# Kernel tuning notes

Measured on AMD Instinct MI355X. Metric: run time of the kernel, lower is better.

## Reference

```python
import jax, jax.numpy as jnp
import numpy as np

EPS = 1e-5

def _layer_norm(x, gamma, beta):
    m = jnp.mean(x, axis=-1, keepdims=True)
    v = jnp.mean(jnp.square(x - m), axis=-1, keepdims=True)
    return (x - m) * jax.lax.rsqrt(v + EPS) * gamma + beta

def setup_inputs() -> dict:
    key = jax.random.key(0)
    ks = jax.random.split(key, 6)
    B, D, H = 4096, 1024, 1024
    s = 1.0 / np.sqrt(H)
    return {
        "inputs": jax.random.normal(ks[0], (B, D), jnp.float32),
        "hx": jax.random.normal(ks[1], (B, H), jnp.float32),
        "cx": jax.random.normal(ks[2], (B, H), jnp.float32),
        "w_ih": jax.random.uniform(ks[3], (4 * H, D), jnp.float32, -s, s),
        "w_hh": jax.random.uniform(ks[4], (4 * H, H), jnp.float32, -s, s),
        "b_hh": jax.random.uniform(ks[5], (4 * H,), jnp.float32, -s, s),
        "g_ih": jnp.ones((4 * H,), jnp.float32),
        "beta_ih": jnp.zeros((4 * H,), jnp.float32),
        "g_hh": jnp.ones((4 * H,), jnp.float32),
        "beta_hh": jnp.zeros((4 * H,), jnp.float32),
        "g_ho": jnp.ones((H,), jnp.float32),
        "beta_ho": jnp.zeros((H,), jnp.float32),
    }

def reference(inputs, hx, cx, w_ih, w_hh, b_hh, g_ih, beta_ih, g_hh, beta_hh, g_ho, beta_ho):
    # i2h: [B, 4H] (no input bias used in original forward)
    i2h = inputs @ w_ih.T
    h2h = hx @ w_hh.T + b_hh
    gates = _layer_norm(i2h, g_ih, beta_ih) + _layer_norm(h2h, g_hh, beta_hh)
    i, f, o, g = jnp.split(gates, 4, axis=1)  # torch chunk order: i, f, o, g
    cy = jax.nn.sigmoid(f) * cx + jax.nn.sigmoid(i) * jnp.tanh(g)
    hy = jax.nn.sigmoid(o) * _layer_norm(jnp.tanh(cy), g_ho, beta_ho)
    # Dropout(0.1) is identity in eval / deterministic reference
    return hy, cy
```

## Files before the change

kernel.cpp:

```cpp
#include <hip/hip_runtime.h>
#include <hip/hip_bf16.h>
#include <stdint.h>

typedef __attribute__((ext_vector_type(8))) short bf16x8;
typedef __attribute__((ext_vector_type(4))) float f32x4;

#define LN_EPS 1e-5f

__device__ inline unsigned f2bf(float f) {
    unsigned u = __builtin_bit_cast(unsigned, f);
    u += 0x7fffu + ((u >> 16) & 1u);
    return u >> 16;
}
__device__ inline float bf2f(unsigned u) {
    return __builtin_bit_cast(float, u << 16);
}
__device__ inline float sigf(float x) {
    return 1.0f / (1.0f + __expf(-x));
}
__device__ inline float tanh_fast(float x) {
    return __builtin_fmaf(2.0f, 1.0f / (1.0f + __expf(-2.0f * x)), -1.0f);
}
__device__ inline float wred(float v) {
#pragma unroll
    for (int o = 32; o > 0; o >>= 1) v += __shfl_xor(v, o);
    return v;
}
__device__ inline void gload_lds16(const void* g, void* l) {
    __builtin_amdgcn_global_load_lds(
        (const __attribute__((address_space(1))) void*)g,
        (__attribute__((address_space(3))) void*)l, 16, 0, 0);
}

__global__ __launch_bounds__(256) void cast_all(
    const float4* __restrict__ s0, ushort4* __restrict__ d0, int n0,
    const float4* __restrict__ s1, ushort4* __restrict__ d1, int n1,
    const float4* __restrict__ s2, ushort4* __restrict__ d2, int n2,
    const float4* __restrict__ s3, ushort4* __restrict__ d3, int n3)
{
    int j = blockIdx.x * blockDim.x + threadIdx.x;
    const float4* s; ushort4* d;
    if (j < n0) { s = s0; d = d0; }
    else {
        j -= n0;
        if (j < n1) { s = s1; d = d1; }
        else {
            j -= n1;
            if (j < n2) { s = s2; d = d2; }
            else {
                j -= n2;
                if (j >= n3) return;
                s = s3; d = d3;
            }
        }
    }
    float4 v = s[j];
    ushort4 o;
    o.x = (unsigned short)f2bf(v.x); o.y = (unsigned short)f2bf(v.y);
    o.z = (unsigned short)f2bf(v.z); o.w = (unsigned short)f2bf(v.w);
    d[j] = o;
}

#define GNT 32

__global__ __launch_bounds__(512) void gemm8p(
    const short* __restrict__ Aa, const short* __restrict__ Ba, unsigned short* __restrict__ Ca,
    const short* __restrict__ Ab, const short* __restrict__ Bb, unsigned short* __restrict__ Cb,
    const float* __restrict__ Bias,
    float2* __restrict__ P,
    int N, int K, int Bn)
{
    __shared__ __attribute__((aligned(16))) short lds[66048];
    short* ldsA = lds;
    short* ldsB = lds + 32768;
    float* biasLds = (float*)(lds + 65536);

    const int gx = gridDim.x;
    int bid = blockIdx.y * gx + blockIdx.x;
    const int cpx = (gx * gridDim.y) >> 3;
    int swz = (bid & 7) * cpx + (bid >> 3);
    const int by = swz / gx;
    const int bx = swz - by * gx;
    const int brow = by * 256, bcol = bx * 256;

    const int t    = threadIdx.x;
    const int lane = t & 63, w = t >> 6;
    const int wr = w >> 2, wc = w & 3;
    const int lr = lane & 15, kc = lane >> 4;

    const int ci0 = t, ci1 = t + 512;
    const int r0 = ci0 >> 2, l0 = (ci0 & 3) ^ ((r0 >> 1) & 3);
    const int r1 = ci1 >> 2, l1 = (ci1 & 3) ^ ((r1 >> 1) & 3);
    const int gA0 = (brow + r0) * K + l0 * 8;
    const int gA1 = (brow + r1) * K + l1 * 8;
    const int gB0 = (bcol + r0) * K + l0 * 8;
    const int gB1 = (bcol + r1) * K + l1 * 8;
    const int d0 = ci0 * 8, d1 = ci1 * 8;

#define STAGE_A(PA, u) { const int so_ = ((u) & 3) * 8192; \
    gload_lds16((PA) + gA0 + (u) * 32, ldsA + so_ + d0);   \
    gload_lds16((PA) + gA1 + (u) * 32, ldsA + so_ + d1); }
#define STAGE_B(PB, u) { const int so_ = ((u) & 3) * 8192; \
    gload_lds16((PB) + gB0 + (u) * 32, ldsB + so_ + d0);   \
    gload_lds16((PB) + gB1 + (u) * 32, ldsB + so_ + d1); }

    int offW[8], offX[4];
#pragma unroll
    for (int f = 0; f < 8; ++f) {
        int r = wr * 128 + f * 16 + lr;
        offW[f] = r * 32 + ((kc ^ ((r >> 1) & 3)) * 8);
    }
#pragma unroll
    for (int n = 0; n < 4; ++n) {
        int r = wc * 64 + n * 16 + lr;
        offX[n] = r * 32 + ((kc ^ ((r >> 1) & 3)) * 8);
    }

    if (t < 64) gload_lds16(Bias + bcol + t * 4, biasLds + t * 4);

    STAGE_A(Aa, 0); STAGE_B(Ba, 0); STAGE_A(Aa, 1); STAGE_B(Ba, 1); STAGE_A(Aa, 2);
    asm volatile("s_waitcnt vmcnt(6)" ::: "memory");
    __builtin_amdgcn_s_barrier();

    for (int zz = 0; zz < 2; ++zz) {
        const short* A = zz ? Ab : Aa;
        const short* B = zz ? Bb : Ba;
        unsigned short* C = zz ? Cb : Ca;

        f32x4 acc[8][4];
#pragma unroll
        for (int i = 0; i < 8; ++i)
#pragma unroll
            for (int j = 0; j < 4; ++j)
                acc[i][j] = (f32x4){0.f, 0.f, 0.f, 0.f};

#pragma unroll 4
        for (int T = 0; T < GNT; ++T) {
            const int so = (T & 3) * 8192;
            bf16x8 w0, w1, w2, w3, x0, x1, x2, x3;

            w0 = *(const bf16x8*)&ldsB[so + offW[0]];
            w1 = *(const bf16x8*)&ldsB[so + offW[1]];
            w2 = *(const bf16x8*)&ldsB[so + offW[2]];
            w3 = *(const bf16x8*)&ldsB[so + offW[3]];
            x0 = *(const bf16x8*)&ldsA[so + offX[0]];
            x1 = *(const bf16x8*)&ldsA[so + offX[1]];
            x2 = *(const bf16x8*)&ldsA[so + offX[2]];
            x3 = *(const bf16x8*)&ldsA[so + offX[3]];
            if (T + 2 < GNT) STAGE_B(B, T + 2);
            __builtin_amdgcn_s_barrier();
            asm volatile("s_waitcnt lgkmcnt(0)" ::: "memory");
            __builtin_amdgcn_sched_barrier(0);
            __builtin_amdgcn_s_setprio(1);
            acc[0][0] = __builtin_amdgcn_mfma_f32_16x16x32_bf16(w0, x0, acc[0][0], 0, 0, 0);
            acc[0][1] = __builtin_amdgcn_mfma_f32_16x16x32_bf16(w0, x1, acc[0][1], 0, 0, 0);
            acc[0][2] = __builtin_amdgcn_mfma_f32_16x16x32_bf16(w0, x2, acc[0][2], 0, 0, 0);
            acc[0][3] = __builtin_amdgcn_mfma_f32_16x16x32_bf16(w0, x3, acc[0][3], 0, 0, 0);
            acc[1][0] = __builtin_amdgcn_mfma_f32_16x16x32_bf16(w1, x0, acc[1][0], 0, 0, 0);
            acc[1][1] = __builtin_amdgcn_mfma_f32_16x16x32_bf16(w1, x1, acc[1][1], 0, 0, 0);
            acc[1][2] = __builtin_amdgcn_mfma_f32_16x16x32_bf16(w1, x2, acc[1][2], 0, 0, 0);
            acc[1][3] = __builtin_amdgcn_mfma_f32_16x16x32_bf16(w1, x3, acc[1][3], 0, 0, 0);
            acc[2][0] = __builtin_amdgcn_mfma_f32_16x16x32_bf16(w2, x0, acc[2][0], 0, 0, 0);
            acc[2][1] = __builtin_amdgcn_mfma_f32_16x16x32_bf16(w2, x1, acc[2][1], 0, 0, 0);
            acc[2][2] = __builtin_amdgcn_mfma_f32_16x16x32_bf16(w2, x2, acc[2][2], 0, 0, 0);
            acc[2][3] = __builtin_amdgcn_mfma_f32_16x16x32_bf16(w2, x3, acc[2][3], 0, 0, 0);
            acc[3][0] = __builtin_amdgcn_mfma_f32_16x16x32_bf16(w3, x0, acc[3][0], 0, 0, 0);
            acc[3][1] = __builtin_amdgcn_mfma_f32_16x16x32_bf16(w3, x1, acc[3][1], 0, 0, 0);
            acc[3][2] = __builtin_amdgcn_mfma_f32_16x16x32_bf16(w3, x2, acc[3][2], 0, 0, 0);
            acc[3][3] = __builtin_amdgcn_mfma_f32_16x16x32_bf16(w3, x3, acc[3][3], 0, 0, 0);
            __builtin_amdgcn_s_setprio(0);
            __builtin_amdgcn_s_barrier();

            w0 = *(const bf16x8*)&ldsB[so + offW[4]];
            w1 = *(const bf16x8*)&ldsB[so + offW[5]];
            w2 = *(const bf16x8*)&ldsB[so + offW[6]];
            w3 = *(const bf16x8*)&ldsB[so + offW[7]];
            if (T + 3 < GNT) STAGE_A(A, T + 3);
            __builtin_amdgcn_s_barrier();
            asm volatile("s_waitcnt lgkmcnt(0)" ::: "memory");
            __builtin_amdgcn_sched_barrier(0);
            __builtin_amdgcn_s_setprio(1);
            acc[4][0] = __builtin_amdgcn_mfma_f32_16x16x32_bf16(w0, x0, acc[4][0], 0, 0, 0);
            acc[4][1] = __builtin_amdgcn_mfma_f32_16x16x32_bf16(w0, x1, acc[4][1], 0, 0, 0);
            acc[4][2] = __builtin_amdgcn_mfma_f32_16x16x32_bf16(w0, x2, acc[4][2], 0, 0, 0);
            acc[4][3] = __builtin_amdgcn_mfma_f32_16x16x32_bf16(w0, x3, acc[4][3], 0, 0, 0);
            acc[5][0] = __builtin_amdgcn_mfma_f32_16x16x32_bf16(w1, x0, acc[5][0], 0, 0, 0);
            acc[5][1] = __builtin_amdgcn_mfma_f32_16x16x32_bf16(w1, x1, acc[5][1], 0, 0, 0);
            acc[5][2] = __builtin_amdgcn_mfma_f32_16x16x32_bf16(w1, x2, acc[5][2], 0, 0, 0);
            acc[5][3] = __builtin_amdgcn_mfma_f32_16x16x32_bf16(w1, x3, acc[5][3], 0, 0, 0);
            acc[6][0] = __builtin_amdgcn_mfma_f32_16x16x32_bf16(w2, x0, acc[6][0], 0, 0, 0);
            acc[6][1] = __builtin_amdgcn_mfma_f32_16x16x32_bf16(w2, x1, acc[6][1], 0, 0, 0);
            acc[6][2] = __builtin_amdgcn_mfma_f32_16x16x32_bf16(w2, x2, acc[6][2], 0, 0, 0);
            acc[6][3] = __builtin_amdgcn_mfma_f32_16x16x32_bf16(w2, x3, acc[6][3], 0, 0, 0);
            acc[7][0] = __builtin_amdgcn_mfma_f32_16x16x32_bf16(w3, x0, acc[7][0], 0, 0, 0);
            acc[7][1] = __builtin_amdgcn_mfma_f32_16x16x32_bf16(w3, x1, acc[7][1], 0, 0, 0);
            acc[7][2] = __builtin_amdgcn_mfma_f32_16x16x32_bf16(w3, x2, acc[7][2], 0, 0, 0);
            acc[7][3] = __builtin_amdgcn_mfma_f32_16x16x32_bf16(w3, x3, acc[7][3], 0, 0, 0);
            __builtin_amdgcn_s_setprio(0);
            if (T < GNT - 3)      { asm volatile("s_waitcnt vmcnt(6)" ::: "memory"); }
            else if (T == GNT - 3){ asm volatile("s_waitcnt vmcnt(4)" ::: "memory"); }
            else if (T == GNT - 2){ asm volatile("s_waitcnt vmcnt(0)" ::: "memory"); }
            __builtin_amdgcn_s_barrier();
        }

        if (zz == 0) {
            STAGE_A(Ab, 0); STAGE_B(Bb, 0); STAGE_A(Ab, 1); STAGE_B(Bb, 1); STAGE_A(Ab, 2);
        }

        const int gc0 = bcol + wr * 128 + kc * 4;
        const int mr0 = brow + wc * 64 + lr;
        const int bl0 = wr * 32 + kc;

        float s[4] = {0.f, 0.f, 0.f, 0.f}, q[4] = {0.f, 0.f, 0.f, 0.f};
#pragma unroll
        for (int f = 0; f < 8; ++f) {
            float4 b4;
            if (zz) b4 = ((const float4*)biasLds)[bl0 + f * 4];
            else    b4 = (float4){0.f, 0.f, 0.f, 0.f};
#pragma unroll
            for (int n = 0; n < 4; ++n) {
                float v0 = acc[f][n][0] + b4.x;
                float v1 = acc[f][n][1] + b4.y;
                float v2 = acc[f][n][2] + b4.z;
                float v3 = acc[f][n][3] + b4.w;
                unsigned u0 = f2bf(v0), u1 = f2bf(v1), u2 = f2bf(v2), u3 = f2bf(v3);
                float e0 = bf2f(u0), e1 = bf2f(u1), e2 = bf2f(u2), e3 = bf2f(u3);
                s[n] += (e0 + e1) + (e2 + e3);
                q[n] += (e0 * e0 + e1 * e1) + (e2 * e2 + e3 * e3);
                uint2 pk; pk.x = u0 | (u1 << 16); pk.y = u2 | (u3 << 16);
                *reinterpret_cast<uint2*>(&C[(size_t)(mr0 + n * 16) * N + gc0 + f * 16]) = pk;
            }
        }
#pragma unroll
        for (int n = 0; n < 4; ++n) {
            s[n] += __shfl_xor(s[n], 16); s[n] += __shfl_xor(s[n], 32);
            q[n] += __shfl_xor(q[n], 16); q[n] += __shfl_xor(q[n], 32);
        }
        if (kc == 0) {
#pragma unroll
            for (int n = 0; n < 4; ++n) {
                float2 pr; pr.x = s[n]; pr.y = q[n];
                P[(size_t)(zz * Bn + mr0 + n * 16) * 32 + bx * 2 + wr] = pr;
            }
        }

        if (zz == 0) {
            asm volatile("s_waitcnt vmcnt(0)" ::: "memory");
            __builtin_amdgcn_s_barrier();
        }
    }
#undef STAGE_A
#undef STAGE_B
}

__global__ __launch_bounds__(256) void ln_lstm(
    const unsigned short* __restrict__ i2h,
    const unsigned short* __restrict__ h2h,
    const float* __restrict__ cx,
    const float2* __restrict__ P,
    const float* __restrict__ g_ih, const float* __restrict__ be_ih,
    const float* __restrict__ g_hh, const float* __restrict__ be_hh,
    const float* __restrict__ g_ho, const float* __restrict__ be_ho,
    float* __restrict__ hy, float* __restrict__ cy, int H, int B)
{
    const int b = blockIdx.x;
    const int t = threadIdx.x;
    const int lane = t & 63;
    const int wave = t >> 6;
    const int H4 = 4 * H;
    const int h0 = t * 4;

    const unsigned short* xi = i2h + (size_t)b * H4;
    const unsigned short* xh = h2h + (size_t)b * H4;

    __shared__ float red[4][2];
    __shared__ float st[4];

    if (wave == 0) {
        const int half = lane >> 5;
        float2 v = P[((size_t)half * B + b) * 32 + (lane & 31)];
        v.x += __shfl_xor(v.x, 1);  v.y += __shfl_xor(v.y, 1);
        v.x += __shfl_xor(v.x, 2);  v.y += __shfl_xor(v.y, 2);
        v.x += __shfl_xor(v.x, 4);  v.y += __shfl_xor(v.y, 4);
        v.x += __shfl_xor(v.x, 8);  v.y += __shfl_xor(v.y, 8);
        v.x += __shfl_xor(v.x, 16); v.y += __shfl_xor(v.y, 16);
        if ((lane & 31) == 0) {
            const float inv4H = 1.0f / (float)H4;
            float m = v.x * inv4H;
            float r = rsqrtf(v.y * inv4H - m * m + LN_EPS);
            st[half * 2]     = m;
            st[half * 2 + 1] = r;
        }
    }
    __syncthreads();
    const float mI = st[0], rI = st[1], mH = st[2], rH = st[3];

    float gate[4][4];
#pragma unroll
    for (int q = 0; q < 4; ++q) {
        const int j = q * H + h0;
        ushort4 vi = *reinterpret_cast<const ushort4*>(&xi[j]);
        ushort4 vh = *reinterpret_cast<const ushort4*>(&xh[j]);
        float4 gi = *reinterpret_cast<const float4*>(&g_ih[j]);
        float4 bi = *reinterpret_cast<const float4*>(&be_ih[j]);
        float4 gh = *reinterpret_cast<const float4*>(&g_hh[j]);
        float4 bh = *reinterpret_cast<const float4*>(&be_hh[j]);
        gate[q][0] = (bf2f(vi.x) - mI) * rI * gi.x + bi.x + (bf2f(vh.x) - mH) * rH * gh.x + bh.x;
        gate[q][1] = (bf2f(vi.y) - mI) * rI * gi.y + bi.y + (bf2f(vh.y) - mH) * rH * gh.y + bh.y;
        gate[q][2] = (bf2f(vi.z) - mI) * rI * gi.z + bi.z + (bf2f(vh.z) - mH) * rH * gh.z + bh.z;
        gate[q][3] = (bf2f(vi.w) - mI) * rI * gi.w + bi.w + (bf2f(vh.w) - mH) * rH * gh.w + bh.w;
    }

    float4 cxv = *reinterpret_cast<const float4*>(&cx[(size_t)b * H + h0]);
    float cvals[4] = {cxv.x, cxv.y, cxv.z, cxv.w};
    float tv[4], ov[4];
    float s2 = 0.f, q2 = 0.f;
    float4 cyv;
#pragma unroll
    for (int k = 0; k < 4; ++k) {
        float c = sigf(gate[1][k]) * cvals[k] + sigf(gate[0][k]) * tanh_fast(gate[3][k]);
        ((float*)&cyv)[k] = c;
        float tc = tanh_fast(c);
        tv[k] = tc; ov[k] = sigf(gate[2][k]);
        s2 += tc; q2 += tc * tc;
    }
    *reinterpret_cast<float4*>(&cy[(size_t)b * H + h0]) = cyv;

    s2 = wred(s2); q2 = wred(q2);
    if (lane == 0) { red[wave][0] = s2; red[wave][1] = q2; }
    __syncthreads();
    float S2 = red[0][0] + red[1][0] + red[2][0] + red[3][0];
    float Q2 = red[0][1] + red[1][1] + red[2][1] + red[3][1];
    const float invH = 1.0f / (float)H;
    float mt = S2 * invH;
    float rt = rsqrtf(Q2 * invH - mt * mt + LN_EPS);

    float4 go = *reinterpret_cast<const float4*>(&g_ho[h0]);
    float4 bo = *reinterpret_cast<const float4*>(&be_ho[h0]);
    float4 hyv;
    hyv.x = ov[0] * ((tv[0] - mt) * rt * go.x + bo.x);
    hyv.y = ov[1] * ((tv[1] - mt) * rt * go.y + bo.y);
    hyv.z = ov[2] * ((tv[2] - mt) * rt * go.z + bo.z);
    hyv.w = ov[3] * ((tv[3] - mt) * rt * go.w + bo.w);
    *reinterpret_cast<float4*>(&hy[(size_t)b * H + h0]) = hyv;
}

extern "C" void kernel_launch(void* const* d_in, const int* in_sizes, int n_in,
                              void* d_out, int out_size, void* d_ws, size_t ws_size,
                              hipStream_t stream) {
    const float* inputs  = (const float*)d_in[0];
    const float* hx      = (const float*)d_in[1];
    const float* cx      = (const float*)d_in[2];
    const float* w_ih    = (const float*)d_in[3];
    const float* w_hh    = (const float*)d_in[4];
    const float* b_hh    = (const float*)d_in[5];
    const float* g_ih    = (const float*)d_in[6];
    const float* beta_ih = (const float*)d_in[7];
    const float* g_hh    = (const float*)d_in[8];
    const float* beta_hh = (const float*)d_in[9];
    const float* g_ho    = (const float*)d_in[10];
    const float* beta_ho = (const float*)d_in[11];

    const int H  = in_sizes[10];
    const int B  = in_sizes[1] / H;
    const int D  = in_sizes[0] / B;
    const int H4 = 4 * H;

    uint8_t* ws = (uint8_t*)d_ws;
    size_t off = 0;
    short* Abf  = (short*)(ws + off); off += (size_t)B * D * 2;
    short* Hbf  = (short*)(ws + off); off += (size_t)B * H * 2;
    short* Wih  = (short*)(ws + off); off += (size_t)H4 * D * 2;
    short* Whh  = (short*)(ws + off); off += (size_t)H4 * H * 2;
    unsigned short* i2hb = (unsigned short*)(ws + off); off += (size_t)B * H4 * 2;
    unsigned short* h2hb = (unsigned short*)(ws + off); off += (size_t)B * H4 * 2;
    float2* P   = (float2*)(ws + off); off += (size_t)2 * B * 32 * sizeof(float2);

    float* hy  = (float*)d_out;
    float* cyo = (float*)d_out + (size_t)B * H;

    {
        const int n0 = (B * D) / 4, n1 = (B * H) / 4, n2 = (H4 * D) / 4, n3 = (H4 * H) / 4;
        const int tot = n0 + n1 + n2 + n3;
        cast_all<<<(tot + 255) / 256, 256, 0, stream>>>(
            (const float4*)inputs, (ushort4*)Abf, n0,
            (const float4*)hx,     (ushort4*)Hbf, n1,
            (const float4*)w_ih,   (ushort4*)Wih, n2,
            (const float4*)w_hh,   (ushort4*)Whh, n3);
    }

    {
        dim3 grid(H4 / 256, B / 256, 1);
        gemm8p<<<grid, 512, 0, stream>>>(Abf, Wih, i2hb, Hbf, Whh, h2hb, b_hh, P, H4, D, B);
    }

    ln_lstm<<<B, 256, 0, stream>>>(i2hb, h2hb, cx, P,
                                   g_ih, beta_ih, g_hh, beta_hh, g_ho, beta_ho,
                                   hy, cyo, H, B);
}
```

Baseline: 134.6 us.

## Split dual GEMM across grid z and fold bias into padded K column

```diff
diff --git a/kernel.cpp b/kernel.cpp
--- a/kernel.cpp
+++ b/kernel.cpp
@@ -6,6 +6,8 @@
 typedef __attribute__((ext_vector_type(4))) float f32x4;
 
 #define LN_EPS 1e-5f
+#define KP 1056
+#define GNT 33
 
 __device__ inline unsigned f2bf(float f) {
     unsigned u = __builtin_bit_cast(unsigned, f);
@@ -32,55 +34,71 @@
         (__attribute__((address_space(3))) void*)l, 16, 0, 0);
 }
 
-__global__ __launch_bounds__(256) void cast_all(
-    const float4* __restrict__ s0, ushort4* __restrict__ d0, int n0,
-    const float4* __restrict__ s1, ushort4* __restrict__ d1, int n1,
-    const float4* __restrict__ s2, ushort4* __restrict__ d2, int n2,
-    const float4* __restrict__ s3, ushort4* __restrict__ d3, int n3)
+__global__ __launch_bounds__(256) void cast_aug(
+    const float* __restrict__ inputs, const float* __restrict__ hx,
+    const float* __restrict__ w_ih,   const float* __restrict__ w_hh,
+    const float* __restrict__ b_hh,
+    unsigned short* __restrict__ Abf, unsigned short* __restrict__ Hbf,
+    unsigned short* __restrict__ Wih, unsigned short* __restrict__ Whh)
 {
+    const int CPR = 132;
+    const int PERREG = 4096 * CPR;
     int j = blockIdx.x * blockDim.x + threadIdx.x;
-    const float4* s; ushort4* d;
-    if (j < n0) { s = s0; d = d0; }
-    else {
-        j -= n0;
-        if (j < n1) { s = s1; d = d1; }
-        else {
-            j -= n1;
-            if (j < n2) { s = s2; d = d2; }
-            else {
-                j -= n2;
-                if (j >= n3) return;
-                s = s3; d = d3;
-            }
+    const int r = j / PERREG;
+    if (r >= 4) return;
+    const int rem = j - r * PERREG;
+    const int row = rem / CPR;
+    const int c8  = rem - row * CPR;
+
+    const float* src; unsigned short* dst;
+    switch (r) {
+        case 0: src = inputs; dst = Abf; break;
+        case 1: src = hx;     dst = Hbf; break;
+        case 2: src = w_ih;   dst = Wih; break;
+        default: src = w_hh;  dst = Whh; break;
+    }
+
+    uint4 v;
+    if (c8 < 128) {
+        const float4* sp = reinterpret_cast<const float4*>(src + (size_t)row * 1024 + c8 * 8);
+        float4 a = sp[0], b = sp[1];
+        v.x = f2bf(a.x) | (f2bf(a.y) << 16);
+        v.y = f2bf(a.z) | (f2bf(a.w) << 16);
+        v.z = f2bf(b.x) | (f2bf(b.y) << 16);
+        v.w = f2bf(b.z) | (f2bf(b.w) << 16);
+    } else {
+        v.x = v.y = v.z = v.w = 0u;
+        if (c8 == 128) {
+            if (r == 1) v.x = 0x3F80u;
+            else if (r == 3) v.x = f2bf(b_hh[row]);
         }
     }
-    float4 v = s[j];
-    ushort4 o;
-    o.x = (unsigned short)f2bf(v.x); o.y = (unsigned short)f2bf(v.y);
-    o.z = (unsigned short)f2bf(v.z); o.w = (unsigned short)f2bf(v.w);
-    d[j] = o;
-}
-
-#define GNT 32
+    *reinterpret_cast<uint4*>(dst + (size_t)row * KP + c8 * 8) = v;
+}
 
 __global__ __launch_bounds__(512) void gemm8p(
-    const short* __restrict__ Aa, const short* __restrict__ Ba, unsigned short* __restrict__ Ca,
-    const short* __restrict__ Ab, const short* __restrict__ Bb, unsigned short* __restrict__ Cb,
-    const float* __restrict__ Bias,
+    const unsigned short* __restrict__ Aa, const unsigned short* __restrict__ Ba, unsigned short* __restrict__ Ca,
+    const unsigned short* __restrict__ Ab, const unsigned short* __restrict__ Bb, unsigned short* __restrict__ Cb,
     float2* __restrict__ P,
-    int N, int K, int Bn)
+    int N, int Bn)
 {
-    __shared__ __attribute__((aligned(16))) short lds[66048];
+    __shared__ __attribute__((aligned(16))) short lds[65536];
     short* ldsA = lds;
     short* ldsB = lds + 32768;
-    float* biasLds = (float*)(lds + 65536);
-
-    const int gx = gridDim.x;
-    int bid = blockIdx.y * gx + blockIdx.x;
-    const int cpx = (gx * gridDim.y) >> 3;
+
+    const int gx  = gridDim.x;
+    const int gxy = gx * gridDim.y;
+    int bid = (blockIdx.z * gridDim.y + blockIdx.y) * gx + blockIdx.x;
+    const int cpx = (gxy * gridDim.z) >> 3;
     int swz = (bid & 7) * cpx + (bid >> 3);
-    const int by = swz / gx;
-    const int bx = swz - by * gx;
+    const int z  = swz / gxy;
+    const int r2 = swz - z * gxy;
+    const int by = r2 / gx;
+    const int bx = r2 - by * gx;
+
+    const unsigned short* __restrict__ A = z ? Ab : Aa;
+    const unsigned short* __restrict__ B = z ? Bb : Ba;
+    unsigned short* __restrict__ C = z ? Cb : Ca;
     const int brow = by * 256, bcol = bx * 256;
 
     const int t    = threadIdx.x;
@@ -91,18 +109,18 @@
     const int ci0 = t, ci1 = t + 512;
     const int r0 = ci0 >> 2, l0 = (ci0 & 3) ^ ((r0 >> 1) & 3);
     const int r1 = ci1 >> 2, l1 = (ci1 & 3) ^ ((r1 >> 1) & 3);
-    const int gA0 = (brow + r0) * K + l0 * 8;
-    const int gA1 = (brow + r1) * K + l1 * 8;
-    const int gB0 = (bcol + r0) * K + l0 * 8;
-    const int gB1 = (bcol + r1) * K + l1 * 8;
+    const int gA0 = (brow + r0) * KP + l0 * 8;
+    const int gA1 = (brow + r1) * KP + l1 * 8;
+    const int gB0 = (bcol + r0) * KP + l0 * 8;
+    const int gB1 = (bcol + r1) * KP + l1 * 8;
     const int d0 = ci0 * 8, d1 = ci1 * 8;
 
-#define STAGE_A(PA, u) { const int so_ = ((u) & 3) * 8192; \
-    gload_lds16((PA) + gA0 + (u) * 32, ldsA + so_ + d0);   \
-    gload_lds16((PA) + gA1 + (u) * 32, ldsA + so_ + d1); }
-#define STAGE_B(PB, u) { const int so_ = ((u) & 3) * 8192; \
-    gload_lds16((PB) + gB0 + (u) * 32, ldsB + so_ + d0);   \
-    gload_lds16((PB) + gB1 + (u) * 32, ldsB + so_ + d1); }
+#define STAGE_A(u) { const int so_ = ((u) & 3) * 8192; \
+    gload_lds16(A + gA0 + (u) * 32, ldsA + so_ + d0);  \
+    gload_lds16(A + gA1 + (u) * 32, ldsA + so_ + d1); }
+#define STAGE_B(u) { const int so_ = ((u) & 3) * 8192; \
+    gload_lds16(B + gB0 + (u) * 32, ldsB + so_ + d0);  \
+    gload_lds16(B + gB1 + (u) * 32, ldsB + so_ + d1); }
 
     int offW[8], offX[4];
 #pragma unroll
@@ -116,137 +134,113 @@
         offX[n] = r * 32 + ((kc ^ ((r >> 1) & 3)) * 8);
     }
 
-    if (t < 64) gload_lds16(Bias + bcol + t * 4, biasLds + t * 4);
-
-    STAGE_A(Aa, 0); STAGE_B(Ba, 0); STAGE_A(Aa, 1); STAGE_B(Ba, 1); STAGE_A(Aa, 2);
+    f32x4 acc[8][4];
+#pragma unroll
+    for (int i = 0; i < 8; ++i)
+#pragma unroll
+        for (int j = 0; j < 4; ++j)
+            acc[i][j] = (f32x4){0.f, 0.f, 0.f, 0.f};
+
+    STAGE_A(0); STAGE_B(0); STAGE_A(1); STAGE_B(1); STAGE_A(2);
     asm volatile("s_waitcnt vmcnt(6)" ::: "memory");
     __builtin_amdgcn_s_barrier();
 
-    for (int zz = 0; zz < 2; ++zz) {
-        const short* A = zz ? Ab : Aa;
-        const short* B = zz ? Bb : Ba;
-        unsigned short* C = zz ? Cb : Ca;
-
-        f32x4 acc[8][4];
-#pragma unroll
-        for (int i = 0; i < 8; ++i)
-#pragma unroll
-            for (int j = 0; j < 4; ++j)
-                acc[i][j] = (f32x4){0.f, 0.f, 0.f, 0.f};
-
 #pragma unroll 4
-        for (int T = 0; T < GNT; ++T) {
-            const int so = (T & 3) * 8192;
-            bf16x8 w0, w1, w2, w3, x0, x1, x2, x3;
-
-            w0 = *(const bf16x8*)&ldsB[so + offW[0]];
-            w1 = *(const bf16x8*)&ldsB[so + offW[1]];
-            w2 = *(const bf16x8*)&ldsB[so + offW[2]];
-            w3 = *(const bf16x8*)&ldsB[so + offW[3]];
-            x0 = *(const bf16x8*)&ldsA[so + offX[0]];
-            x1 = *(const bf16x8*)&ldsA[so + offX[1]];
-            x2 = *(const bf16x8*)&ldsA[so + offX[2]];
-            x3 = *(const bf16x8*)&ldsA[so + offX[3]];
-            if (T + 2 < GNT) STAGE_B(B, T + 2);
-            __builtin_amdgcn_s_barrier();
-            asm volatile("s_waitcnt lgkmcnt(0)" ::: "memory");
-            __builtin_amdgcn_sched_barrier(0);
-            __builtin_amdgcn_s_setprio(1);
-            acc[0][0] = __builtin_amdgcn_mfma_f32_16x16x32_bf16(w0, x0, acc[0][0], 0, 0, 0);
-            acc[0][1] = __builtin_amdgcn_mfma_f32_16x16x32_bf16(w0, x1, acc[0][1], 0, 0, 0);
-            acc[0][2] = __builtin_amdgcn_mfma_f32_16x16x32_bf16(w0, x2, acc[0][2], 0, 0, 0);
-            acc[0][3] = __builtin_amdgcn_mfma_f32_16x16x32_bf16(w0, x3, acc[0][3], 0, 0, 0);
-            acc[1][0] = __builtin_amdgcn_mfma_f32_16x16x32_bf16(w1, x0, acc[1][0], 0, 0, 0);
-            acc[1][1] = __builtin_amdgcn_mfma_f32_16x16x32_bf16(w1, x1, acc[1][1], 0, 0, 0);
-            acc[1][2] = __builtin_amdgcn_mfma_f32_16x16x32_bf16(w1, x2, acc[1][2], 0, 0, 0);
-            acc[1][3] = __builtin_amdgcn_mfma_f32_16x16x32_bf16(w1, x3, acc[1][3], 0, 0, 0);
-            acc[2][0] = __builtin_amdgcn_mfma_f32_16x16x32_bf16(w2, x0, acc[2][0], 0, 0, 0);
-            acc[2][1] = __builtin_amdgcn_mfma_f32_16x16x32_bf16(w2, x1, acc[2][1], 0, 0, 0);
-            acc[2][2] = __builtin_amdgcn_mfma_f32_16x16x32_bf16(w2, x2, acc[2][2], 0, 0, 0);
-            acc[2][3] = __builtin_amdgcn_mfma_f32_16x16x32_bf16(w2, x3, acc[2][3], 0, 0, 0);
-            acc[3][0] = __builtin_amdgcn_mfma_f32_16x16x32_bf16(w3, x0, acc[3][0], 0, 0, 0);
-            acc[3][1] = __builtin_amdgcn_mfma_f32_16x16x32_bf16(w3, x1, acc[3][1], 0, 0, 0);
-            acc[3][2] = __builtin_amdgcn_mfma_f32_16x16x32_bf16(w3, x2, acc[3][2], 0, 0, 0);
-            acc[3][3] = __builtin_amdgcn_mfma_f32_16x16x32_bf16(w3, x3, acc[3][3], 0, 0, 0);
-            __builtin_amdgcn_s_setprio(0);
-            __builtin_amdgcn_s_barrier();
-
-            w0 = *(const bf16x8*)&ldsB[so + offW[4]];
-            w1 = *(const bf16x8*)&ldsB[so + offW[5]];
-            w2 = *(const bf16x8*)&ldsB[so + offW[6]];
-            w3 = *(const bf16x8*)&ldsB[so + offW[7]];
-            if (T + 3 < GNT) STAGE_A(A, T + 3);
-            __builtin_amdgcn_s_barrier();
-            asm volatile("s_waitcnt lgkmcnt(0)" ::: "memory");
-            __builtin_amdgcn_sched_barrier(0);
-            __builtin_amdgcn_s_setprio(1);
-            acc[4][0] = __builtin_amdgcn_mfma_f32_16x16x32_bf16(w0, x0, acc[4][0], 0, 0, 0);
-            acc[4][1] = __builtin_amdgcn_mfma_f32_16x16x32_bf16(w0, x1, acc[4][1], 0, 0, 0);
-            acc[4][2] = __builtin_amdgcn_mfma_f32_16x16x32_bf16(w0, x2, acc[4][2], 0, 0, 0);
-            acc[4][3] = __builtin_amdgcn_mfma_f32_16x16x32_bf16(w0, x3, acc[4][3], 0, 0, 0);
-            acc[5][0] = __builtin_amdgcn_mfma_f32_16x16x32_bf16(w1, x0, acc[5][0], 0, 0, 0);
-            acc[5][1] = __builtin_amdgcn_mfma_f32_16x16x32_bf16(w1, x1, acc[5][1], 0, 0, 0);
-            acc[5][2] = __builtin_amdgcn_mfma_f32_16x16x32_bf16(w1, x2, acc[5][2], 0, 0, 0);
-            acc[5][3] = __builtin_amdgcn_mfma_f32_16x16x32_bf16(w1, x3, acc[5][3], 0, 0, 0);
-            acc[6][0] = __builtin_amdgcn_mfma_f32_16x16x32_bf16(w2, x0, acc[6][0], 0, 0, 0);
-            acc[6][1] = __builtin_amdgcn_mfma_f32_16x16x32_bf16(w2, x1, acc[6][1], 0, 0, 0);
-            acc[6][2] = __builtin_amdgcn_mfma_f32_16x16x32_bf16(w2, x2, acc[6][2], 0, 0, 0);
-            acc[6][3] = __builtin_amdgcn_mfma_f32_16x16x32_bf16(w2, x3, acc[6][3], 0, 0, 0);
-            acc[7][0] = __builtin_amdgcn_mfma_f32_16x16x32_bf16(w3, x0, acc[7][0], 0, 0, 0);
-            acc[7][1] = __builtin_amdgcn_mfma_f32_16x16x32_bf16(w3, x1, acc[7][1], 0, 0, 0);
-            acc[7][2] = __builtin_amdgcn_mfma_f32_16x16x32_bf16(w3, x2, acc[7][2], 0, 0, 0);
-            acc[7][3] = __builtin_amdgcn_mfma_f32_16x16x32_bf16(w3, x3, acc[7][3], 0, 0, 0);
-            __builtin_amdgcn_s_setprio(0);
-            if (T < GNT - 3)      { asm volatile("s_waitcnt vmcnt(6)" ::: "memory"); }
-            else if (T == GNT - 3){ asm volatile("s_waitcnt vmcnt(4)" ::: "memory"); }
-            else if (T == GNT - 2){ asm volatile("s_waitcnt vmcnt(0)" ::: "memory"); }
-            __builtin_amdgcn_s_barrier();
+    for (int T = 0; T < GNT; ++T) {
+        const int so = (T & 3) * 8192;
+        bf16x8 w0, w1, w2, w3, x0, x1, x2, x3;
+
+        w0 = *(const bf16x8*)&ldsB[so + offW[0]];
+        w1 = *(const bf16x8*)&ldsB[so + offW[1]];
+        w2 = *(const bf16x8*)&ldsB[so + offW[2]];
+        w3 = *(const bf16x8*)&ldsB[so + offW[3]];
+        x0 = *(const bf16x8*)&ldsA[so + offX[0]];
+        x1 = *(const bf16x8*)&ldsA[so + offX[1]];
+        x2 = *(const bf16x8*)&ldsA[so + offX[2]];
+        x3 = *(const bf16x8*)&ldsA[so + offX[3]];
+        if (T + 2 < GNT) STAGE_B(T + 2);
+        __builtin_amdgcn_s_barrier();
+        asm volatile("s_waitcnt lgkmcnt(0)" ::: "memory");
+        __builtin_amdgcn_sched_barrier(0);
+        __builtin_amdgcn_s_setprio(1);
+        acc[0][0] = __builtin_amdgcn_mfma_f32_16x16x32_bf16(w0, x0, acc[0][0], 0, 0, 0);
+        acc[0][1] = __builtin_amdgcn_mfma_f32_16x16x32_bf16(w0, x1, acc[0][1], 0, 0, 0);
+        acc[0][2] = __builtin_amdgcn_mfma_f32_16x16x32_bf16(w0, x2, acc[0][2], 0, 0, 0);
+        acc[0][3] = __builtin_amdgcn_mfma_f32_16x16x32_bf16(w0, x3, acc[0][3], 0, 0, 0);
+        acc[1][0] = __builtin_amdgcn_mfma_f32_16x16x32_bf16(w1, x0, acc[1][0], 0, 0, 0);
+        acc[1][1] = __builtin_amdgcn_mfma_f32_16x16x32_bf16(w1, x1, acc[1][1], 0, 0, 0);
+        acc[1][2] = __builtin_amdgcn_mfma_f32_16x16x32_bf16(w1, x2, acc[1][2], 0, 0, 0);
+        acc[1][3] = __builtin_amdgcn_mfma_f32_16x16x32_bf16(w1, x3, acc[1][3], 0, 0, 0);
+        acc[2][0] = __builtin_amdgcn_mfma_f32_16x16x32_bf16(w2, x0, acc[2][0], 0, 0, 0);
+        acc[2][1] = __builtin_amdgcn_mfma_f32_16x16x32_bf16(w2, x1, acc[2][1], 0, 0, 0);
+        acc[2][2] = __builtin_amdgcn_mfma_f32_16x16x32_bf16(w2, x2, acc[2][2], 0, 0, 0);
+        acc[2][3] = __builtin_amdgcn_mfma_f32_16x16x32_bf16(w2, x3, acc[2][3], 0, 0, 0);
+        acc[3][0] = __builtin_amdgcn_mfma_f32_16x16x32_bf16(w3, x0, acc[3][0], 0, 0, 0);
+        acc[3][1] = __builtin_amdgcn_mfma_f32_16x16x32_bf16(w3, x1, acc[3][1], 0, 0, 0);
+        acc[3][2] = __builtin_amdgcn_mfma_f32_16x16x32_bf16(w3, x2, acc[3][2], 0, 0, 0);
+        acc[3][3] = __builtin_amdgcn_mfma_f32_16x16x32_bf16(w3, x3, acc[3][3], 0, 0, 0);
+        __builtin_amdgcn_s_setprio(0);
+        __builtin_amdgcn_s_barrier();
+
+        w0 = *(const bf16x8*)&ldsB[so + offW[4]];
+        w1 = *(const bf16x8*)&ldsB[so + offW[5]];
+        w2 = *(const bf16x8*)&ldsB[so + offW[6]];
+        w3 = *(const bf16x8*)&ldsB[so + offW[7]];
+        if (T + 3 < GNT) STAGE_A(T + 3);
+        __builtin_amdgcn_s_barrier();
+        asm volatile("s_waitcnt lgkmcnt(0)" ::: "memory");
+        __builtin_amdgcn_sched_barrier(0);
+        __builtin_amdgcn_s_setprio(1);
+        acc[4][0] = __builtin_amdgcn_mfma_f32_16x16x32_bf16(w0, x0, acc[4][0], 0, 0, 0);
+        acc[4][1] = __builtin_amdgcn_mfma_f32_16x16x32_bf16(w0, x1, acc[4][1], 0, 0, 0);
+        acc[4][2] = __builtin_amdgcn_mfma_f32_16x16x32_bf16(w0, x2, acc[4][2], 0, 0, 0);
+        acc[4][3] = __builtin_amdgcn_mfma_f32_16x16x32_bf16(w0, x3, acc[4][3], 0, 0, 0);
+        acc[5][0] = __builtin_amdgcn_mfma_f32_16x16x32_bf16(w1, x0, acc[5][0], 0, 0, 0);
+        acc[5][1] = __builtin_amdgcn_mfma_f32_16x16x32_bf16(w1, x1, acc[5][1], 0, 0, 0);
+        acc[5][2] = __builtin_amdgcn_mfma_f32_16x16x32_bf16(w1, x2, acc[5][2], 0, 0, 0);
+        acc[5][3] = __builtin_amdgcn_mfma_f32_16x16x32_bf16(w1, x3, acc[5][3], 0, 0, 0);
+        acc[6][0] = __builtin_amdgcn_mfma_f32_16x16x32_bf16(w2, x0, acc[6][0], 0, 0, 0);
+        acc[6][1] = __builtin_amdgcn_mfma_f32_16x16x32_bf16(w2, x1, acc[6][1], 0, 0, 0);
+        acc[6][2] = __builtin_amdgcn_mfma_f32_16x16x32_bf16(w2, x2, acc[6][2], 0, 0, 0);
+        acc[6][3] = __builtin_amdgcn_mfma_f32_16x16x32_bf16(w2, x3, acc[6][3], 0, 0, 0);
+        acc[7][0] = __builtin_amdgcn_mfma_f32_16x16x32_bf16(w3, x0, acc[7][0], 0, 0, 0);
+        acc[7][1] = __builtin_amdgcn_mfma_f32_16x16x32_bf16(w3, x1, acc[7][1], 0, 0, 0);
+        acc[7][2] = __builtin_amdgcn_mfma_f32_16x16x32_bf16(w3, x2, acc[7][2], 0, 0, 0);
+        acc[7][3] = __builtin_amdgcn_mfma_f32_16x16x32_bf16(w3, x3, acc[7][3], 0, 0, 0);
+        __builtin_amdgcn_s_setprio(0);
+        if (T < GNT - 3)      { asm volatile("s_waitcnt vmcnt(6)" ::: "memory"); }
+        else if (T == GNT - 3){ asm volatile("s_waitcnt vmcnt(4)" ::: "memory"); }
+        else if (T == GNT - 2){ asm volatile("s_waitcnt vmcnt(0)" ::: "memory"); }
+        __builtin_amdgcn_s_barrier();
+    }
+
+    const int gc0 = bcol + wr * 128 + kc * 4;
+    const int mr0 = brow + wc * 64 + lr;
+
+    float s[4] = {0.f, 0.f, 0.f, 0.f}, q[4] = {0.f, 0.f, 0.f, 0.f};
+#pragma unroll
+    for (int f = 0; f < 8; ++f) {
+#pragma unroll
+        for (int n = 0; n < 4; ++n) {
+            float a0 = acc[f][n][0], a1 = acc[f][n][1];
+            float a2 = acc[f][n][2], a3 = acc[f][n][3];
+            s[n] += (a0 + a1) + (a2 + a3);
+            q[n] += __builtin_fmaf(a0, a0, a1 * a1) + __builtin_fmaf(a2, a2, a3 * a3);
+            unsigned u0 = f2bf(a0), u1 = f2bf(a1), u2 = f2bf(a2), u3 = f2bf(a3);
+            uint2 pk; pk.x = u0 | (u1 << 16); pk.y = u2 | (u3 << 16);
+            *reinterpret_cast<uint2*>(&C[(size_t)(mr0 + n * 16) * N + gc0 + f * 16]) = pk;
         }
-
-        if (zz == 0) {
-            STAGE_A(Ab, 0); STAGE_B(Bb, 0); STAGE_A(Ab, 1); STAGE_B(Bb, 1); STAGE_A(Ab, 2);
-        }
-
-        const int gc0 = bcol + wr * 128 + kc * 4;
-        const int mr0 = brow + wc * 64 + lr;
-        const int bl0 = wr * 32 + kc;
-
-        float s[4] = {0.f, 0.f, 0.f, 0.f}, q[4] = {0.f, 0.f, 0.f, 0.f};
-#pragma unroll
-        for (int f = 0; f < 8; ++f) {
-            float4 b4;
-            if (zz) b4 = ((const float4*)biasLds)[bl0 + f * 4];
-            else    b4 = (float4){0.f, 0.f, 0.f, 0.f};
-#pragma unroll
-            for (int n = 0; n < 4; ++n) {
-                float v0 = acc[f][n][0] + b4.x;
-                float v1 = acc[f][n][1] + b4.y;
-                float v2 = acc[f][n][2] + b4.z;
-                float v3 = acc[f][n][3] + b4.w;
-                unsigned u0 = f2bf(v0), u1 = f2bf(v1), u2 = f2bf(v2), u3 = f2bf(v3);
-                float e0 = bf2f(u0), e1 = bf2f(u1), e2 = bf2f(u2), e3 = bf2f(u3);
-                s[n] += (e0 + e1) + (e2 + e3);
-                q[n] += (e0 * e0 + e1 * e1) + (e2 * e2 + e3 * e3);
-                uint2 pk; pk.x = u0 | (u1 << 16); pk.y = u2 | (u3 << 16);
-                *reinterpret_cast<uint2*>(&C[(size_t)(mr0 + n * 16) * N + gc0 + f * 16]) = pk;
-            }
-        }
+    }
+#pragma unroll
+    for (int n = 0; n < 4; ++n) {
+        s[n] += __shfl_xor(s[n], 16); s[n] += __shfl_xor(s[n], 32);
+        q[n] += __shfl_xor(q[n], 16); q[n] += __shfl_xor(q[n], 32);
+    }
+    if (kc == 0) {
 #pragma unroll
         for (int n = 0; n < 4; ++n) {
-            s[n] += __shfl_xor(s[n], 16); s[n] += __shfl_xor(s[n], 32);
-            q[n] += __shfl_xor(q[n], 16); q[n] += __shfl_xor(q[n], 32);
-        }
-        if (kc == 0) {
-#pragma unroll
-            for (int n = 0; n < 4; ++n) {
-                float2 pr; pr.x = s[n]; pr.y = q[n];
-                P[(size_t)(zz * Bn + mr0 + n * 16) * 32 + bx * 2 + wr] = pr;
-            }
-        }
-
-        if (zz == 0) {
-            asm volatile("s_waitcnt vmcnt(0)" ::: "memory");
-            __builtin_amdgcn_s_barrier();
+            float2 pr; pr.x = s[n]; pr.y = q[n];
+            P[(size_t)(z * Bn + mr0 + n * 16) * 32 + bx * 2 + wr] = pr;
         }
     }
 #undef STAGE_A
@@ -363,15 +357,14 @@
 
     const int H  = in_sizes[10];
     const int B  = in_sizes[1] / H;
-    const int D  = in_sizes[0] / B;
     const int H4 = 4 * H;
 
     uint8_t* ws = (uint8_t*)d_ws;
     size_t off = 0;
-    short* Abf  = (short*)(ws + off); off += (size_t)B * D * 2;
-    short* Hbf  = (short*)(ws + off); off += (size_t)B * H * 2;
-    short* Wih  = (short*)(ws + off); off += (size_t)H4 * D * 2;
-    short* Whh  = (short*)(ws + off); off += (size_t)H4 * H * 2;
+    unsigned short* Abf = (unsigned short*)(ws + off); off += (size_t)B * KP * 2;
+    unsigned short* Hbf = (unsigned short*)(ws + off); off += (size_t)B * KP * 2;
+    unsigned short* Wih = (unsigned short*)(ws + off); off += (size_t)H4 * KP * 2;
+    unsigned short* Whh = (unsigned short*)(ws + off); off += (size_t)H4 * KP * 2;
     unsigned short* i2hb = (unsigned short*)(ws + off); off += (size_t)B * H4 * 2;
     unsigned short* h2hb = (unsigned short*)(ws + off); off += (size_t)B * H4 * 2;
     float2* P   = (float2*)(ws + off); off += (size_t)2 * B * 32 * sizeof(float2);
@@ -380,18 +373,14 @@
     float* cyo = (float*)d_out + (size_t)B * H;
 
     {
-        const int n0 = (B * D) / 4, n1 = (B * H) / 4, n2 = (H4 * D) / 4, n3 = (H4 * H) / 4;
-        const int tot = n0 + n1 + n2 + n3;
-        cast_all<<<(tot + 255) / 256, 256, 0, stream>>>(
-            (const float4*)inputs, (ushort4*)Abf, n0,
-            (const float4*)hx,     (ushort4*)Hbf, n1,
-            (const float4*)w_ih,   (ushort4*)Wih, n2,
-            (const float4*)w_hh,   (ushort4*)Whh, n3);
+        const int tot = 4 * 4096 * 132;
+        cast_aug<<<(tot + 255) / 256, 256, 0, stream>>>(
+            inputs, hx, w_ih, w_hh, b_hh, Abf, Hbf, Wih, Whh);
     }
 
     {
-        dim3 grid(H4 / 256, B / 256, 1);
-        gemm8p<<<grid, 512, 0, stream>>>(Abf, Wih, i2hb, Hbf, Whh, h2hb, b_hh, P, H4, D, B);
+        dim3 grid(H4 / 256, B / 256, 2);
+        gemm8p<<<grid, 512, 0, stream>>>(Abf, Wih, i2hb, Hbf, Whh, h2hb, P, H4, B);
     }
 
     ln_lstm<<<B, 256, 0, stream>>>(i2hb, h2hb, cx, P,
```

Result: faster. 123.7 us (median of 3 runs) (-8.1%).
